# Performance work log

Measured on AMD Instinct MI355X. Metric: run time of the kernel, lower is better.

## Reference

```python
import jax, jax.numpy as jnp
import numpy as np

B, N, F_IN, F_OUT, E = 8, 2048, 512, 256, 5
ALPHA = 0.2  # leaky relu slope
NEG = -9e15


def setup_inputs() -> dict:
    key = jax.random.key(0)
    ks = jax.random.split(key, 11)
    s_in = 1.0 / np.sqrt(F_IN)
    s_out = 1.0 / np.sqrt(F_OUT)
    s_e = 1.0 / np.sqrt(E)
    return {
        "feat": jax.random.normal(ks[0], (B, N, F_IN), jnp.float32),
        "adj": jax.random.randint(ks[1], (B, N, N), 0, 2, jnp.int32),
        "W": jax.random.normal(ks[2], (F_IN, F_OUT), jnp.float32) * s_in,
        "W_1": jax.random.normal(ks[3], (F_IN, F_OUT), jnp.float32) * s_in,
        "W_2": jax.random.normal(ks[4], (F_IN, F_OUT), jnp.float32) * s_in,
        "a_1": jax.random.normal(ks[5], (F_OUT, 1), jnp.float32) * s_out,
        "a_2": jax.random.normal(ks[6], (F_OUT, 1), jnp.float32) * s_out,
        "a_12": jax.random.normal(ks[7], (F_OUT, F_OUT), jnp.float32) * s_out,
        "L_w": jax.random.normal(ks[8], (E, F_IN), jnp.float32) * s_in,
        "R_w": jax.random.normal(ks[9], (E, F_IN), jnp.float32) * s_in,
        "B_w": jax.random.normal(ks[10], (F_OUT, E, E), jnp.float32) * s_e,
    }


def reference(feat, adj, W, W_1, W_2, a_1, a_2, a_12, L_w, R_w, B_w):
    # --- attention ---
    h = jnp.einsum('bnf,fd->bnd', feat, W)                 # [B,N,D]
    Ax = jnp.einsum('bnd,do->bno', h, a_1)[..., 0]         # [B,N] (score of target)
    Ay = jnp.einsum('bnd,do->bno', h, a_2)[..., 0]         # [B,N] (score of source)
    A_xy = jnp.einsum('bid,de,bje->bij', h, a_12, h)       # [B,N,N] bilinear term
    logits = Ax[:, None, :] + Ay[:, :, None] + A_xy        # [B,N,N]
    e = jnp.where(logits > 0, logits, ALPHA * logits)      # leaky relu
    e = jnp.where(adj > 0, e, NEG)
    attention = jax.nn.softmax(e, axis=-1)                 # dropout p=0 / eval -> identity
    # --- aggregate ---
    feat_agg = jnp.einsum('bij,bjf->bif', attention, feat) # [B,N,F_IN]
    # --- update ---
    h_1 = jnp.einsum('bnf,fd->bnd', feat, W_1)
    h_2 = jnp.einsum('bnf,fd->bnd', feat_agg, W_2)
    e1 = jnp.einsum('bnf,ef->bne', feat, L_w)              # [B,N,E]
    e2 = jnp.einsum('bnf,ef->bne', feat_agg, R_w)          # [B,N,E]
    h_12 = jnp.einsum('bni,oij,bnj->bno', e1, B_w, e2)     # [B,N,F_OUT]
    return h_1 + h_2 + h_12  # activation=None -> identity
```

## Files before the change

### kernel.cpp

```cpp
#include <hip/hip_runtime.h>
#include <hip/hip_bf16.h>

#define BB 8
#define NN 2048
#define FIN 512
#define FOUT 256
#define EE 5
#define ALPHA_ 0.2f
#define NEGV -9e15f
#define JW 512

typedef __hip_bfloat16 bf16;
typedef __bf16 bf16x8 __attribute__((ext_vector_type(8)));
typedef float f32x4 __attribute__((ext_vector_type(4)));
typedef unsigned long long u64;

__device__ __forceinline__ float bf2f(bf16 x) { return __bfloat162float(x); }
__device__ __forceinline__ bf16 f2bf(float x) { return __float2bfloat16(x); }

__global__ void split_f32_bf16(const float* __restrict__ in,
                               bf16* __restrict__ hi, bf16* __restrict__ lo) {
    long i = ((long)blockIdx.x * blockDim.x + threadIdx.x) * 8;
    float4 a = *(const float4*)(&in[i]);
    float4 b = *(const float4*)(&in[i + 4]);
    float x[8] = { a.x, a.y, a.z, a.w, b.x, b.y, b.z, b.w };
    bf16 th[8], tl[8];
    for (int k = 0; k < 8; k++) {
        th[k] = f2bf(x[k]);
        tl[k] = f2bf(x[k] - bf2f(th[k]));
    }
    *(uint4*)(&hi[i]) = *(const uint4*)th;
    *(uint4*)(&lo[i]) = *(const uint4*)tl;
}

__global__ void pack_adj(const int* __restrict__ adj, u64* __restrict__ adjm) {
    long wid = (((long)blockIdx.x * 256) + threadIdx.x) >> 6;
    int lane = threadIdx.x & 63;
    long base = wid * 256;
    for (int c = 0; c < 4; c++) {
        int a = adj[base + c * 64 + lane];
        u64 m = __ballot(a > 0);
        if (lane == 0) adjm[base / 64 + c] = m;
    }
}

__global__ void transpose_split(const float* __restrict__ in,
                                bf16* __restrict__ hi, bf16* __restrict__ lo,
                                int R, int C) {
    __shared__ bf16 th[32][33], tl[32][33];
    int c0 = blockIdx.x * 32, r0 = blockIdx.y * 32;
    int x = threadIdx.x, y = threadIdx.y;
    for (int k = 0; k < 4; k++) {
        int r = y + k * 8;
        float f = in[(long)(r0 + r) * C + c0 + x];
        bf16 h = f2bf(f);
        th[r][x] = h;
        tl[r][x] = f2bf(f - bf2f(h));
    }
    __syncthreads();
    for (int k = 0; k < 4; k++) {
        int r = y + k * 8;
        hi[(long)(c0 + r) * R + r0 + x] = th[x][r];
        lo[(long)(c0 + r) * R + r0 + x] = tl[x][r];
    }
}

__global__ void transpose_f32_bf16(const float* __restrict__ in, bf16* __restrict__ out,
                                   int R, int C, long sin_b, long sout_b) {
    __shared__ bf16 tile[32][33];
    long bi = (long)blockIdx.z * sin_b;
    long bo = (long)blockIdx.z * sout_b;
    int c0 = blockIdx.x * 32, r0 = blockIdx.y * 32;
    int x = threadIdx.x, y = threadIdx.y;
    for (int k = 0; k < 4; k++) {
        int r = y + k * 8;
        tile[r][x] = f2bf(in[bi + (long)(r0 + r) * C + c0 + x]);
    }
    __syncthreads();
    for (int k = 0; k < 4; k++) {
        int r = y + k * 8;
        out[bo + (long)(c0 + r) * R + r0 + x] = tile[x][r];
    }
}

__global__ __launch_bounds__(256) void gemm_bt_split(
        const bf16* __restrict__ Ah, const bf16* __restrict__ Al,
        const bf16* __restrict__ Bh, const bf16* __restrict__ Bl,
        bf16* __restrict__ Chi, bf16* __restrict__ Clo,
        const float* __restrict__ bias, int Nn, int K) {
    __shared__ alignas(16) bf16 Ash[128 * 32], Asl[128 * 32];
    __shared__ alignas(16) bf16 Bsh[128 * 32], Bsl[128 * 32];
    int tid = threadIdx.x;
    int lane = tid & 63, ww = tid >> 6;
    int wm = ww >> 1, wn = ww & 1;
    int quad = lane >> 4, l16 = lane & 15;
    int m0 = blockIdx.x * 128, n0 = blockIdx.y * 128;
    f32x4 acc[4][4] = {};
    for (int k0 = 0; k0 < K; k0 += 32) {
        for (int i = 0; i < 2; i++) {
            int idx = tid + i * 256;
            int row = idx >> 2, seg = idx & 3;
            long ao = (long)(m0 + row) * K + k0 + seg * 8;
            long bo = (long)(n0 + row) * K + k0 + seg * 8;
            int so = row * 32 + seg * 8;
            *(uint4*)(&Ash[so]) = *(const uint4*)(&Ah[ao]);
            *(uint4*)(&Asl[so]) = *(const uint4*)(&Al[ao]);
            *(uint4*)(&Bsh[so]) = *(const uint4*)(&Bh[bo]);
            *(uint4*)(&Bsl[so]) = *(const uint4*)(&Bl[bo]);
        }
        __syncthreads();
        bf16x8 afh[4], afl[4], bfh[4], bfl[4];
        for (int mi = 0; mi < 4; mi++) {
            int so = (wm * 64 + mi * 16 + l16) * 32 + quad * 8;
            afh[mi] = *(const bf16x8*)(&Ash[so]);
            afl[mi] = *(const bf16x8*)(&Asl[so]);
        }
        for (int ni = 0; ni < 4; ni++) {
            int so = (wn * 64 + ni * 16 + l16) * 32 + quad * 8;
            bfh[ni] = *(const bf16x8*)(&Bsh[so]);
            bfl[ni] = *(const bf16x8*)(&Bsl[so]);
        }
        for (int mi = 0; mi < 4; mi++)
            for (int ni = 0; ni < 4; ni++) {
                acc[mi][ni] = __builtin_amdgcn_mfma_f32_16x16x32_bf16(afh[mi], bfh[ni], acc[mi][ni], 0, 0, 0);
                acc[mi][ni] = __builtin_amdgcn_mfma_f32_16x16x32_bf16(afh[mi], bfl[ni], acc[mi][ni], 0, 0, 0);
                acc[mi][ni] = __builtin_amdgcn_mfma_f32_16x16x32_bf16(afl[mi], bfh[ni], acc[mi][ni], 0, 0, 0);
            }
        __syncthreads();
    }
    for (int mi = 0; mi < 4; mi++)
        for (int ni = 0; ni < 4; ni++) {
            int col = n0 + wn * 64 + ni * 16 + l16;
            float bv = bias ? bias[col] : 0.f;
            for (int r = 0; r < 4; r++) {
                int row = m0 + wm * 64 + mi * 16 + quad * 4 + r;
                float v = acc[mi][ni][r] + bv;
                bf16 h = f2bf(v);
                Chi[(long)row * Nn + col] = h;
                Clo[(long)row * Nn + col] = f2bf(v - bf2f(h));
            }
        }
}

__global__ __launch_bounds__(256) void gemm_bt(
        const bf16* __restrict__ A, const bf16* __restrict__ Bt,
        bf16* __restrict__ C, int Nn, int K, long sA, long sB, long sC) {
    __shared__ alignas(16) bf16 As[128 * 32];
    __shared__ alignas(16) bf16 Bs[128 * 32];
    const bf16* Ab = A + (long)blockIdx.z * sA;
    const bf16* Bb = Bt + (long)blockIdx.z * sB;
    bf16* Cb = C + (long)blockIdx.z * sC;
    int tid = threadIdx.x;
    int lane = tid & 63, ww = tid >> 6;
    int wm = ww >> 1, wn = ww & 1;
    int quad = lane >> 4, l16 = lane & 15;
    int m0 = blockIdx.x * 128, n0 = blockIdx.y * 128;
    f32x4 acc[4][4] = {};
    for (int k0 = 0; k0 < K; k0 += 32) {
        for (int i = 0; i < 2; i++) {
            int idx = tid + i * 256;
            int row = idx >> 2, seg = idx & 3;
            int so = row * 32 + seg * 8;
            *(uint4*)(&As[so]) =
                *(const uint4*)(&Ab[(long)(m0 + row) * K + k0 + seg * 8]);
            *(uint4*)(&Bs[so]) =
                *(const uint4*)(&Bb[(long)(n0 + row) * K + k0 + seg * 8]);
        }
        __syncthreads();
        bf16x8 af[4], bfr[4];
        for (int mi = 0; mi < 4; mi++)
            af[mi] = *(const bf16x8*)(&As[(wm * 64 + mi * 16 + l16) * 32 + quad * 8]);
        for (int ni = 0; ni < 4; ni++)
            bfr[ni] = *(const bf16x8*)(&Bs[(wn * 64 + ni * 16 + l16) * 32 + quad * 8]);
        for (int mi = 0; mi < 4; mi++)
            for (int ni = 0; ni < 4; ni++)
                acc[mi][ni] = __builtin_amdgcn_mfma_f32_16x16x32_bf16(
                    af[mi], bfr[ni], acc[mi][ni], 0, 0, 0);
        __syncthreads();
    }
    for (int mi = 0; mi < 4; mi++)
        for (int ni = 0; ni < 4; ni++) {
            int col = n0 + wn * 64 + ni * 16 + l16;
            for (int r = 0; r < 4; r++) {
                int row = m0 + wm * 64 + mi * 16 + quad * 4 + r;
                Cb[(long)row * Nn + col] = f2bf(acc[mi][ni][r]);
            }
        }
}

__global__ void ay_kernel(const bf16* __restrict__ hh, const bf16* __restrict__ hl,
                          const float* __restrict__ a2, float* __restrict__ Ay) {
    int lane = threadIdx.x & 63, w = threadIdx.x >> 6;
    long row = (long)blockIdx.x * 4 + w;
    float p = 0.f;
    for (int i = 0; i < 4; i++) {
        int d = i * 64 + lane;
        p += (bf2f(hh[row * FOUT + d]) + bf2f(hl[row * FOUT + d])) * a2[d];
    }
    for (int off = 32; off; off >>= 1) p += __shfl_xor(p, off);
    if (lane == 0) Ay[row] = p;
}

__global__ __launch_bounds__(256) void pass_score(
        const bf16* __restrict__ qh_, const bf16* __restrict__ ql_,
        const bf16* __restrict__ hh_, const bf16* __restrict__ hl_,
        const u64* __restrict__ adjm, const float* __restrict__ Ay,
        float* __restrict__ mpm, float* __restrict__ mpl,
        bf16* __restrict__ P, int b0) {
    __shared__ alignas(16) bf16 Hsh[128 * 32], Hsl[128 * 32];
    __shared__ alignas(16) bf16 pst[4][16 * 128];
    int tid = threadIdx.x;
    int lane = tid & 63, w = tid >> 6;
    int quad = lane >> 4, l16 = lane & 15;
    int bz = blockIdx.z, b = b0 + bz, jz = blockIdx.y;
    int i0 = blockIdx.x * 64 + w * 16;
    long qoff = ((long)b * NN + i0) * FOUT;
    const bf16* hbh = hh_ + ((long)b * NN + (long)jz * JW) * FOUT;
    const bf16* hbl = hl_ + ((long)b * NN + (long)jz * JW) * FOUT;
    const u64* amb = adjm + ((long)b * NN + i0) * (NN / 64) + jz * (JW / 64);
    bf16* pw = pst[w];

    bf16x8 qfh[8], qfl[8];
#pragma unroll
    for (int kk = 0; kk < 8; kk++) {
        qfh[kk] = *(const bf16x8*)(&qh_[qoff + (long)l16 * FOUT + kk * 32 + quad * 8]);
        qfl[kk] = *(const bf16x8*)(&ql_[qoff + (long)l16 * FOUT + kk * 32 + quad * 8]);
    }
    float ay_[4];
#pragma unroll
    for (int r = 0; r < 4; r++) ay_[r] = Ay[(long)b * NN + i0 + quad * 4 + r];

    float m_[4], l_[4];
#pragma unroll
    for (int r = 0; r < 4; r++) { m_[r] = -3.0e38f; l_[r] = 0.f; }

    for (int jc = 0; jc < JW / 128; jc++) {
        f32x4 sacc[8] = {};
#pragma unroll
        for (int kk = 0; kk < 8; kk++) {
            __syncthreads();
#pragma unroll
            for (int i = 0; i < 2; i++) {
                int idx = tid + i * 256;
                int row = idx >> 2, seg = idx & 3;
                long go = (long)(jc * 128 + row) * FOUT + kk * 32 + seg * 8;
                int so = row * 32 + seg * 8;
                *(uint4*)(&Hsh[so]) = *(const uint4*)(&hbh[go]);
                *(uint4*)(&Hsl[so]) = *(const uint4*)(&hbl[go]);
            }
            __syncthreads();
#pragma unroll
            for (int ni = 0; ni < 8; ni++) {
                int so = (ni * 16 + l16) * 32 + quad * 8;
                bf16x8 hfh = *(const bf16x8*)(&Hsh[so]);
                bf16x8 hfl = *(const bf16x8*)(&Hsl[so]);
                sacc[ni] = __builtin_amdgcn_mfma_f32_16x16x32_bf16(qfh[kk], hfh, sacc[ni], 0, 0, 0);
                sacc[ni] = __builtin_amdgcn_mfma_f32_16x16x32_bf16(qfh[kk], hfl, sacc[ni], 0, 0, 0);
                sacc[ni] = __builtin_amdgcn_mfma_f32_16x16x32_bf16(qfl[kk], hfh, sacc[ni], 0, 0, 0);
            }
        }
        u64 am[4][2];
#pragma unroll
        for (int r = 0; r < 4; r++) {
            am[r][0] = amb[(long)(quad * 4 + r) * (NN / 64) + jc * 2 + 0];
            am[r][1] = amb[(long)(quad * 4 + r) * (NN / 64) + jc * 2 + 1];
        }
#pragma unroll
        for (int ni = 0; ni < 8; ni++)
#pragma unroll
            for (int r = 0; r < 4; r++) {
                float v = sacc[ni][r] + ay_[r];
                v = v > 0.f ? v : ALPHA_ * v;
                int bit = (int)((am[r][ni >> 2] >> ((ni * 16 + l16) & 63)) & 1);
                sacc[ni][r] = bit ? v : NEGV;
            }
#pragma unroll
        for (int r = 0; r < 4; r++) {
            float mc = -3.0e38f;
#pragma unroll
            for (int ni = 0; ni < 8; ni++) mc = fmaxf(mc, sacc[ni][r]);
            for (int off = 8; off; off >>= 1) mc = fmaxf(mc, __shfl_xor(mc, off));
            float mnew = fmaxf(m_[r], mc);
            float scale = __expf(m_[r] - mnew);
            float ps = 0.f;
#pragma unroll
            for (int ni = 0; ni < 8; ni++) {
                float p = __expf(sacc[ni][r] - mnew);
                sacc[ni][r] = p;
                ps += p;
            }
            for (int off = 8; off; off >>= 1) ps += __shfl_xor(ps, off);
            l_[r] = l_[r] * scale + ps;
            m_[r] = mnew;
            if (l16 == 0)
                mpm[(((long)bz * 4 + jz) * 4 + jc) * NN + i0 + quad * 4 + r] = mnew;
        }
#pragma unroll
        for (int ni = 0; ni < 8; ni++)
#pragma unroll
            for (int r = 0; r < 4; r++)
                pw[(quad * 4 + r) * 128 + ni * 16 + l16] = f2bf(sacc[ni][r]);
#pragma unroll
        for (int s2 = 0; s2 < 4; s2++) {
            int seg = quad * 4 + s2;
            uint4 v = *(const uint4*)(&pw[l16 * 128 + seg * 8]);
            *(uint4*)(&P[((long)bz * NN + i0 + l16) * NN + jz * JW + jc * 128 + seg * 8]) = v;
        }
    }
    if (l16 == 0)
#pragma unroll
        for (int r = 0; r < 4; r++)
            mpl[((long)bz * 4 + jz) * NN + i0 + quad * 4 + r] = l_[r];
}

__global__ void ml_merge(const float* __restrict__ mpm, const float* __restrict__ mpl,
                         float2* __restrict__ mlfin) {
    long row = (long)blockIdx.x * blockDim.x + threadIdx.x;
    long bz = row / NN, n = row % NN;
    float mw[4];
    float m = -3.0e38f;
    for (int jz = 0; jz < 4; jz++) {
        mw[jz] = mpm[((bz * 4 + jz) * 4 + 3) * NN + n];
        m = fmaxf(m, mw[jz]);
    }
    float l = 0.f;
    for (int jz = 0; jz < 4; jz++)
        l += mpl[(bz * 4 + jz) * NN + n] * __expf(mw[jz] - m);
    mlfin[row] = make_float2(m, 1.f / l);
}

__global__ __launch_bounds__(256) void fixup_p(
        bf16* __restrict__ P, const float* __restrict__ mpm,
        const float2* __restrict__ mlfin) {
    int row = blockIdx.x, bz = blockIdx.y;
    int t = threadIdx.x;
    int jz = t >> 6, jc = (t >> 4) & 3;
    float2 mf = mlfin[(long)bz * NN + row];
    float scale = __expf(mpm[(((long)bz * 4 + jz) * 4 + jc) * NN + row] - mf.x) * mf.y;
    long base = ((long)bz * NN + row) * NN + t * 8;
    uint4 v = *(const uint4*)(&P[base]);
    bf16* pv = (bf16*)&v;
    bf16 o[8];
    for (int k = 0; k < 8; k++) o[k] = f2bf(bf2f(pv[k]) * scale);
    *(uint4*)(&P[base]) = *(const uint4*)o;
}

__global__ void e_kernel(const bf16* __restrict__ X, const float* __restrict__ Wt,
                         float* __restrict__ out) {
    int lane = threadIdx.x & 63, w = threadIdx.x >> 6;
    long row = (long)blockIdx.x * 4 + w;
    uint4 raw = *(const uint4*)(&X[row * FIN + lane * 8]);
    const bf16* xp = (const bf16*)&raw;
    float xv[8];
    for (int i = 0; i < 8; i++) xv[i] = bf2f(xp[i]);
    for (int e = 0; e < EE; e++) {
        float4 w0 = *(const float4*)(&Wt[e * FIN + lane * 8]);
        float4 w1 = *(const float4*)(&Wt[e * FIN + lane * 8 + 4]);
        float p = xv[0] * w0.x + xv[1] * w0.y + xv[2] * w0.z + xv[3] * w0.w
                + xv[4] * w1.x + xv[5] * w1.y + xv[6] * w1.z + xv[7] * w1.w;
        for (int off = 32; off; off >>= 1) p += __shfl_xor(p, off);
        if (lane == 0) out[row * EE + e] = p;
    }
}

__global__ void final_kernel(float* __restrict__ out,
                             const bf16* __restrict__ h1, const bf16* __restrict__ h2,
                             const float* __restrict__ e1, const float* __restrict__ e2,
                             const float* __restrict__ Bw) {
    long row = blockIdx.x;
    int o = threadIdx.x;
    float a[EE], c[EE];
    for (int i = 0; i < EE; i++) { a[i] = e1[row * EE + i]; c[i] = e2[row * EE + i]; }
    const float* bw = Bw + (long)o * EE * EE;
    float acc = 0.f;
    for (int i = 0; i < EE; i++)
        for (int j = 0; j < EE; j++)
            acc += bw[i * EE + j] * a[i] * c[j];
    long idx = row * FOUT + o;
    out[idx] = acc + bf2f(h1[idx]) + bf2f(h2[idx]);
}

extern "C" void kernel_launch(void* const* d_in, const int* in_sizes, int n_in,
                              void* d_out, int out_size, void* d_ws, size_t ws_size,
                              hipStream_t stream) {
    const float* feat = (const float*)d_in[0];
    const int*   adj  = (const int*)d_in[1];
    const float* W    = (const float*)d_in[2];
    const float* W1   = (const float*)d_in[3];
    const float* W2   = (const float*)d_in[4];
    const float* a1   = (const float*)d_in[5];
    const float* a2   = (const float*)d_in[6];
    const float* a12  = (const float*)d_in[7];
    const float* Lw   = (const float*)d_in[8];
    const float* Rw   = (const float*)d_in[9];
    const float* Bw   = (const float*)d_in[10];
    float* out = (float*)d_out;

    char* ws = (char*)d_ws;
    size_t off = 0;
    auto alloc = [&](size_t bytes) {
        char* p = ws + off;
        off += (bytes + 255) & ~(size_t)255;
        return p;
    };
    bf16* WTh  = (bf16*)alloc((size_t)FOUT * FIN * 2);
    bf16* WTl  = (bf16*)alloc((size_t)FOUT * FIN * 2);
    bf16* W1T  = (bf16*)alloc((size_t)FOUT * FIN * 2);
    bf16* W2T  = (bf16*)alloc((size_t)FOUT * FIN * 2);
    bf16* aTh  = (bf16*)alloc((size_t)FOUT * FOUT * 2);
    bf16* aTl  = (bf16*)alloc((size_t)FOUT * FOUT * 2);
    bf16* fh   = (bf16*)alloc((size_t)BB * NN * FIN * 2);
    bf16* fl   = (bf16*)alloc((size_t)BB * NN * FIN * 2);
    bf16* hh   = (bf16*)alloc((size_t)BB * NN * FOUT * 2);
    bf16* hl   = (bf16*)alloc((size_t)BB * NN * FOUT * 2);
    bf16* featT= (bf16*)alloc((size_t)BB * NN * FIN * 2);
    float* Ay  = (float*)alloc((size_t)BB * NN * 4);
    float* mpm = (float*)alloc((size_t)4 * 4 * 4 * NN * 4);
    float* mpl = (float*)alloc((size_t)4 * 4 * NN * 4);
    float2* mlfin = (float2*)alloc((size_t)4 * NN * 8);
    float* e1  = (float*)alloc((size_t)BB * NN * EE * 4);
    float* e2  = (float*)alloc((size_t)BB * NN * EE * 4);
    u64* adjm  = (u64*)alloc((size_t)BB * NN * (NN / 64) * 8);
    bf16* P    = (bf16*)alloc((size_t)4 * NN * NN * 2);
    bf16* qh   = (bf16*)d_out;
    bf16* ql   = qh + (size_t)BB * NN * FOUT;
    bf16* fagg = fl;
    bf16* h1   = hh;
    bf16* h2   = hl;

    dim3 tb(32, 8, 1);
    split_f32_bf16<<<(BB * NN * FIN) / (256 * 8), 256, 0, stream>>>(feat, fh, fl);
    pack_adj<<<(BB * NN * NN) / (256 * 4), 256, 0, stream>>>(adj, adjm);
    transpose_split<<<dim3(FOUT / 32, FIN / 32, 1), tb, 0, stream>>>(W, WTh, WTl, FIN, FOUT);
    transpose_split<<<dim3(FOUT / 32, FOUT / 32, 1), tb, 0, stream>>>(a12, aTh, aTl, FOUT, FOUT);
    transpose_f32_bf16<<<dim3(FOUT / 32, FIN / 32, 1), tb, 0, stream>>>(W1, W1T, FIN, FOUT, 0, 0);
    transpose_f32_bf16<<<dim3(FOUT / 32, FIN / 32, 1), tb, 0, stream>>>(W2, W2T, FIN, FOUT, 0, 0);
    transpose_f32_bf16<<<dim3(FIN / 32, NN / 32, BB), tb, 0, stream>>>(
        feat, featT, NN, FIN, (long)NN * FIN, (long)FIN * NN);
    gemm_bt_split<<<dim3(BB * NN / 128, FOUT / 128, 1), 256, 0, stream>>>(
        fh, fl, WTh, WTl, hh, hl, nullptr, FOUT, FIN);
    ay_kernel<<<BB * NN / 4, 256, 0, stream>>>(hh, hl, a2, Ay);
    gemm_bt_split<<<dim3(BB * NN / 128, FOUT / 128, 1), 256, 0, stream>>>(
        hh, hl, aTh, aTl, qh, ql, a1, FOUT, FOUT);
    for (int g = 0; g < 2; g++) {
        pass_score<<<dim3(NN / 64, 4, 4), 256, 0, stream>>>(
            qh, ql, hh, hl, adjm, Ay, mpm, mpl, P, g * 4);
        ml_merge<<<(4 * NN) / 256, 256, 0, stream>>>(mpm, mpl, mlfin);
        fixup_p<<<dim3(NN, 4, 1), 256, 0, stream>>>(P, mpm, mlfin);
        gemm_bt<<<dim3(NN / 128, FIN / 128, 4), 256, 0, stream>>>(
            P, featT + (size_t)g * 4 * FIN * NN, fagg + (size_t)g * 4 * NN * FIN,
            FIN, NN, (long)NN * NN, (long)FIN * NN, (long)NN * FIN);
    }
    gemm_bt<<<dim3(BB * NN / 128, FOUT / 128, 1), 256, 0, stream>>>(
        fh, W1T, h1, FOUT, FIN, 0, 0, 0);
    gemm_bt<<<dim3(BB * NN / 128, FOUT / 128, 1), 256, 0, stream>>>(
        fagg, W2T, h2, FOUT, FIN, 0, 0, 0);
    e_kernel<<<BB * NN / 4, 256, 0, stream>>>(fh, Lw, e1);
    e_kernel<<<BB * NN / 4, 256, 0, stream>>>(fagg, Rw, e2);
    final_kernel<<<BB * NN, FOUT, 0, stream>>>(out, h1, h2, e1, e2, Bw);
}
```

Baseline: 614.5 us.

## Use async global-to-LDS loads in GEMMs and process all batches in one pass

Replaces register-staged global-to-shared copies in the GEMM and score kernels with global_load_lds direct-to-LDS transfers, which cuts VGPR traffic and instruction count in the load phase. It also removes the two-group batch loop, launching the score, merge, fixup and aggregation kernels once over all 8 batches with larger workspace buffers (P doubles to 8×N×N bf16). This lowers launch count and raises per-launch parallelism, at the cost of more workspace memory. The shared layout stays linear (idx*8 matches row*32+seg*8).

```diff
diff --git a/kernel.cpp b/kernel.cpp
--- a/kernel.cpp
+++ b/kernel.cpp
@@ -17,6 +17,12 @@
 
 __device__ __forceinline__ float bf2f(bf16 x) { return __bfloat162float(x); }
 __device__ __forceinline__ bf16 f2bf(float x) { return __float2bfloat16(x); }
+
+__device__ __forceinline__ void async16(const bf16* g, bf16* l) {
+    __builtin_amdgcn_global_load_lds(
+        (const __attribute__((address_space(1))) void*)g,
+        (__attribute__((address_space(3))) void*)l, 16, 0, 0);
+}
 
 __global__ void split_f32_bf16(const float* __restrict__ in,
                                bf16* __restrict__ hi, bf16* __restrict__ lo) {
@@ -97,16 +103,16 @@
     int m0 = blockIdx.x * 128, n0 = blockIdx.y * 128;
     f32x4 acc[4][4] = {};
     for (int k0 = 0; k0 < K; k0 += 32) {
+#pragma unroll
         for (int i = 0; i < 2; i++) {
             int idx = tid + i * 256;
             int row = idx >> 2, seg = idx & 3;
             long ao = (long)(m0 + row) * K + k0 + seg * 8;
             long bo = (long)(n0 + row) * K + k0 + seg * 8;
-            int so = row * 32 + seg * 8;
-            *(uint4*)(&Ash[so]) = *(const uint4*)(&Ah[ao]);
-            *(uint4*)(&Asl[so]) = *(const uint4*)(&Al[ao]);
-            *(uint4*)(&Bsh[so]) = *(const uint4*)(&Bh[bo]);
-            *(uint4*)(&Bsl[so]) = *(const uint4*)(&Bl[bo]);
+            async16(&Ah[ao], &Ash[idx * 8]);
+            async16(&Al[ao], &Asl[idx * 8]);
+            async16(&Bh[bo], &Bsh[idx * 8]);
+            async16(&Bl[bo], &Bsl[idx * 8]);
         }
         __syncthreads();
         bf16x8 afh[4], afl[4], bfh[4], bfl[4];
@@ -157,14 +163,12 @@
     int m0 = blockIdx.x * 128, n0 = blockIdx.y * 128;
     f32x4 acc[4][4] = {};
     for (int k0 = 0; k0 < K; k0 += 32) {
+#pragma unroll
         for (int i = 0; i < 2; i++) {
             int idx = tid + i * 256;
             int row = idx >> 2, seg = idx & 3;
-            int so = row * 32 + seg * 8;
-            *(uint4*)(&As[so]) =
-                *(const uint4*)(&Ab[(long)(m0 + row) * K + k0 + seg * 8]);
-            *(uint4*)(&Bs[so]) =
-                *(const uint4*)(&Bb[(long)(n0 + row) * K + k0 + seg * 8]);
+            async16(&Ab[(long)(m0 + row) * K + k0 + seg * 8], &As[idx * 8]);
+            async16(&Bb[(long)(n0 + row) * K + k0 + seg * 8], &Bs[idx * 8]);
         }
         __syncthreads();
         bf16x8 af[4], bfr[4];
@@ -206,13 +210,13 @@
         const bf16* __restrict__ hh_, const bf16* __restrict__ hl_,
         const u64* __restrict__ adjm, const float* __restrict__ Ay,
         float* __restrict__ mpm, float* __restrict__ mpl,
-        bf16* __restrict__ P, int b0) {
+        bf16* __restrict__ P) {
     __shared__ alignas(16) bf16 Hsh[128 * 32], Hsl[128 * 32];
     __shared__ alignas(16) bf16 pst[4][16 * 128];
     int tid = threadIdx.x;
     int lane = tid & 63, w = tid >> 6;
     int quad = lane >> 4, l16 = lane & 15;
-    int bz = blockIdx.z, b = b0 + bz, jz = blockIdx.y;
+    int b = blockIdx.z, jz = blockIdx.y;
     int i0 = blockIdx.x * 64 + w * 16;
     long qoff = ((long)b * NN + i0) * FOUT;
     const bf16* hbh = hh_ + ((long)b * NN + (long)jz * JW) * FOUT;
@@ -244,9 +248,8 @@
                 int idx = tid + i * 256;
                 int row = idx >> 2, seg = idx & 3;
                 long go = (long)(jc * 128 + row) * FOUT + kk * 32 + seg * 8;
-                int so = row * 32 + seg * 8;
-                *(uint4*)(&Hsh[so]) = *(const uint4*)(&hbh[go]);
-                *(uint4*)(&Hsl[so]) = *(const uint4*)(&hbl[go]);
+                async16(&hbh[go], &Hsh[idx * 8]);
+                async16(&hbl[go], &Hsl[idx * 8]);
             }
             __syncthreads();
 #pragma unroll
@@ -293,7 +296,7 @@
             l_[r] = l_[r] * scale + ps;
             m_[r] = mnew;
             if (l16 == 0)
-                mpm[(((long)bz * 4 + jz) * 4 + jc) * NN + i0 + quad * 4 + r] = mnew;
+                mpm[(((long)b * 4 + jz) * 4 + jc) * NN + i0 + quad * 4 + r] = mnew;
         }
 #pragma unroll
         for (int ni = 0; ni < 8; ni++)
@@ -304,40 +307,40 @@
         for (int s2 = 0; s2 < 4; s2++) {
             int seg = quad * 4 + s2;
             uint4 v = *(const uint4*)(&pw[l16 * 128 + seg * 8]);
-            *(uint4*)(&P[((long)bz * NN + i0 + l16) * NN + jz * JW + jc * 128 + seg * 8]) = v;
+            *(uint4*)(&P[((long)b * NN + i0 + l16) * NN + jz * JW + jc * 128 + seg * 8]) = v;
         }
     }
     if (l16 == 0)
 #pragma unroll
         for (int r = 0; r < 4; r++)
-            mpl[((long)bz * 4 + jz) * NN + i0 + quad * 4 + r] = l_[r];
+            mpl[((long)b * 4 + jz) * NN + i0 + quad * 4 + r] = l_[r];
 }
 
 __global__ void ml_merge(const float* __restrict__ mpm, const float* __restrict__ mpl,
                          float2* __restrict__ mlfin) {
     long row = (long)blockIdx.x * blockDim.x + threadIdx.x;
-    long bz = row / NN, n = row % NN;
+    long b = row / NN, n = row % NN;
     float mw[4];
     float m = -3.0e38f;
     for (int jz = 0; jz < 4; jz++) {
-        mw[jz] = mpm[((bz * 4 + jz) * 4 + 3) * NN + n];
+        mw[jz] = mpm[((b * 4 + jz) * 4 + 3) * NN + n];
         m = fmaxf(m, mw[jz]);
     }
     float l = 0.f;
     for (int jz = 0; jz < 4; jz++)
-        l += mpl[(bz * 4 + jz) * NN + n] * __expf(mw[jz] - m);
+        l += mpl[(b * 4 + jz) * NN + n] * __expf(mw[jz] - m);
     mlfin[row] = make_float2(m, 1.f / l);
 }
 
 __global__ __launch_bounds__(256) void fixup_p(
         bf16* __restrict__ P, const float* __restrict__ mpm,
         const float2* __restrict__ mlfin) {
-    int row = blockIdx.x, bz = blockIdx.y;
+    int row = blockIdx.x, b = blockIdx.y;
     int t = threadIdx.x;
     int jz = t >> 6, jc = (t >> 4) & 3;
-    float2 mf = mlfin[(long)bz * NN + row];
-    float scale = __expf(mpm[(((long)bz * 4 + jz) * 4 + jc) * NN + row] - mf.x) * mf.y;
-    long base = ((long)bz * NN + row) * NN + t * 8;
+    float2 mf = mlfin[(long)b * NN + row];
+    float scale = __expf(mpm[(((long)b * 4 + jz) * 4 + jc) * NN + row] - mf.x) * mf.y;
+    long base = ((long)b * NN + row) * NN + t * 8;
     uint4 v = *(const uint4*)(&P[base]);
     bf16* pv = (bf16*)&v;
     bf16 o[8];
@@ -415,13 +418,13 @@
     bf16* hl   = (bf16*)alloc((size_t)BB * NN * FOUT * 2);
     bf16* featT= (bf16*)alloc((size_t)BB * NN * FIN * 2);
     float* Ay  = (float*)alloc((size_t)BB * NN * 4);
-    float* mpm = (float*)alloc((size_t)4 * 4 * 4 * NN * 4);
-    float* mpl = (float*)alloc((size_t)4 * 4 * NN * 4);
-    float2* mlfin = (float2*)alloc((size_t)4 * NN * 8);
+    float* mpm = (float*)alloc((size_t)BB * 4 * 4 * NN * 4);
+    float* mpl = (float*)alloc((size_t)BB * 4 * NN * 4);
+    float2* mlfin = (float2*)alloc((size_t)BB * NN * 8);
     float* e1  = (float*)alloc((size_t)BB * NN * EE * 4);
     float* e2  = (float*)alloc((size_t)BB * NN * EE * 4);
     u64* adjm  = (u64*)alloc((size_t)BB * NN * (NN / 64) * 8);
-    bf16* P    = (bf16*)alloc((size_t)4 * NN * NN * 2);
+    bf16* P    = (bf16*)alloc((size_t)BB * NN * NN * 2);
     bf16* qh   = (bf16*)d_out;
     bf16* ql   = qh + (size_t)BB * NN * FOUT;
     bf16* fagg = fl;
@@ -442,15 +445,12 @@
     ay_kernel<<<BB * NN / 4, 256, 0, stream>>>(hh, hl, a2, Ay);
     gemm_bt_split<<<dim3(BB * NN / 128, FOUT / 128, 1), 256, 0, stream>>>(
         hh, hl, aTh, aTl, qh, ql, a1, FOUT, FOUT);
-    for (int g = 0; g < 2; g++) {
-        pass_score<<<dim3(NN / 64, 4, 4), 256, 0, stream>>>(
-            qh, ql, hh, hl, adjm, Ay, mpm, mpl, P, g * 4);
-        ml_merge<<<(4 * NN) / 256, 256, 0, stream>>>(mpm, mpl, mlfin);
-        fixup_p<<<dim3(NN, 4, 1), 256, 0, stream>>>(P, mpm, mlfin);
-        gemm_bt<<<dim3(NN / 128, FIN / 128, 4), 256, 0, stream>>>(
-            P, featT + (size_t)g * 4 * FIN * NN, fagg + (size_t)g * 4 * NN * FIN,
-            FIN, NN, (long)NN * NN, (long)FIN * NN, (long)NN * FIN);
-    }
+    pass_score<<<dim3(NN / 64, 4, BB), 256, 0, stream>>>(
+        qh, ql, hh, hl, adjm, Ay, mpm, mpl, P);
+    ml_merge<<<(BB * NN) / 256, 256, 0, stream>>>(mpm, mpl, mlfin);
+    fixup_p<<<dim3(NN, BB, 1), 256, 0, stream>>>(P, mpm, mlfin);
+    gemm_bt<<<dim3(NN / 128, FIN / 128, BB), 256, 0, stream>>>(
+        P, featT, fagg, FIN, NN, (long)NN * NN, (long)FIN * NN, (long)NN * FIN);
     gemm_bt<<<dim3(BB * NN / 128, FOUT / 128, 1), 256, 0, stream>>>(
         fh, W1T, h1, FOUT, FIN, 0, 0, 0);
     gemm_bt<<<dim3(BB * NN / 128, FOUT / 128, 1), 256, 0, stream>>>(
```

Measured after the change: 552.7 us. 10.1% less time.
